# Optimization experiments

Hardware: AMD Instinct MI355X
Metric: run time of the kernel (lower is better)

The kernel has to match this reference:

```python
import jax, jax.numpy as jnp
import numpy as np

# Orthonormal (integral-normalized) real spherical harmonics, l = 0..3,
# components ordered [Y_0^0, Y_1^{-1..1}, Y_2^{-2..2}, Y_3^{-3..3}],
# with the e3nn/cuEquivariance l=1 ordering (y, z, x).
_C00 = float(0.5 * np.sqrt(1.0 / np.pi))
_C1 = float(np.sqrt(3.0 / (4.0 * np.pi)))
_C2m2 = float(0.5 * np.sqrt(15.0 / np.pi))
_C20 = float(0.25 * np.sqrt(5.0 / np.pi))
_C22 = float(0.25 * np.sqrt(15.0 / np.pi))
_C3m3 = float(0.25 * np.sqrt(35.0 / (2.0 * np.pi)))
_C3m2 = float(0.5 * np.sqrt(105.0 / np.pi))
_C3m1 = float(0.25 * np.sqrt(21.0 / (2.0 * np.pi)))
_C30 = float(0.25 * np.sqrt(7.0 / np.pi))
_C32 = float(0.25 * np.sqrt(105.0 / np.pi))

N_EDGES = 4_000_000


def setup_inputs() -> dict:
    key = jax.random.key(0)
    vectors = jax.random.normal(key, (N_EDGES, 3), dtype=jnp.float32)
    return {"vectors": vectors}


def _sh_l3(vectors):
    # normalize=True: project onto unit sphere first
    v = vectors * jax.lax.rsqrt(jnp.sum(vectors * vectors, axis=-1, keepdims=True))
    x, y, z = v[..., 0], v[..., 1], v[..., 2]
    x2, y2, z2 = x * x, y * y, z * z
    one = jnp.ones_like(x)
    ys = [
        _C00 * one,                       # l=0
        _C1 * y, _C1 * z, _C1 * x,        # l=1 (m=-1,0,1)
        _C2m2 * x * y,                    # l=2, m=-2
        _C2m2 * y * z,                    # l=2, m=-1
        _C20 * (3.0 * z2 - 1.0),          # l=2, m=0
        _C2m2 * x * z,                    # l=2, m=1
        _C22 * (x2 - y2),                 # l=2, m=2
        _C3m3 * y * (3.0 * x2 - y2),      # l=3, m=-3
        _C3m2 * x * y * z,                # l=3, m=-2
        _C3m1 * y * (5.0 * z2 - 1.0),     # l=3, m=-1
        _C30 * z * (5.0 * z2 - 3.0),      # l=3, m=0
        _C3m1 * x * (5.0 * z2 - 1.0),     # l=3, m=1
        _C32 * z * (x2 - y2),             # l=3, m=2
        _C3m3 * x * (x2 - 3.0 * y2),      # l=3, m=3
    ]
    return jnp.stack(ys, axis=-1)  # (..., 16)


def reference(vectors) -> jnp.ndarray:
    return _sh_l3(vectors)
```

## Files before the change

kernel.cpp:

```cpp
#include <hip/hip_runtime.h>

#define C00  0.28209479177387814f
#define C1   0.4886025119029199f
#define C2M2 1.0925484305920792f
#define C20  0.31539156525252005f
#define C22  0.5462742152960396f
#define C3M3 0.5900435899266435f
#define C3M2 2.890611442640554f
#define C3M1 0.4570457994644658f
#define C30  0.3731763325901154f
#define C32  1.445305721320277f

typedef float vfloat4 __attribute__((ext_vector_type(4)));

#define PITCH 260

__global__ __launch_bounds__(256) void sh_l3_kernel(
    const float* __restrict__ v, float* __restrict__ out) {
    __shared__ float sh[16][PITCH];

    const int t = threadIdx.x;
    const unsigned gbase = blockIdx.x * 256u;
    const unsigned edge = gbase + t;

    const float* p = v + 3ull * edge;
    float x = p[0], y = p[1], z = p[2];

    float rinv = rsqrtf(x * x + y * y + z * z);
    x *= rinv; y *= rinv; z *= rinv;

    float x2 = x * x, y2 = y * y, z2 = z * z;

    sh[0][t]  = C00;
    sh[1][t]  = C1 * y;
    sh[2][t]  = C1 * z;
    sh[3][t]  = C1 * x;
    sh[4][t]  = C2M2 * x * y;
    sh[5][t]  = C2M2 * y * z;
    sh[6][t]  = C20 * (3.0f * z2 - 1.0f);
    sh[7][t]  = C2M2 * x * z;
    sh[8][t]  = C22 * (x2 - y2);
    sh[9][t]  = C3M3 * y * (3.0f * x2 - y2);
    sh[10][t] = C3M2 * x * y * z;
    sh[11][t] = C3M1 * y * (5.0f * z2 - 1.0f);
    sh[12][t] = C30 * z * (5.0f * z2 - 3.0f);
    sh[13][t] = C3M1 * x * (5.0f * z2 - 1.0f);
    sh[14][t] = C32 * z * (x2 - y2);
    sh[15][t] = C3M3 * x * (x2 - 3.0f * y2);

    __syncthreads();

    vfloat4* out4 = reinterpret_cast<vfloat4*>(out) + 4ull * gbase;
    #pragma unroll
    for (int k = 0; k < 4; ++k) {
        unsigned idx4 = k * 256u + t;
        unsigned e  = idx4 >> 2;
        unsigned c  = (idx4 & 3u) * 4u;
        vfloat4 w;
        w.x = sh[c + 0][e];
        w.y = sh[c + 1][e];
        w.z = sh[c + 2][e];
        w.w = sh[c + 3][e];
        __builtin_nontemporal_store(w, &out4[idx4]);
    }
}

extern "C" void kernel_launch(void* const* d_in, const int* in_sizes, int n_in,
                              void* d_out, int out_size, void* d_ws, size_t ws_size,
                              hipStream_t stream) {
    const float* v = (const float*)d_in[0];
    float* out = (float*)d_out;
    int n = in_sizes[0] / 3;
    int grid = n / 256;
    sh_l3_kernel<<<grid, 256, 0, stream>>>(v, out);
}
```

Before: 284.7 us.

## Stage input through LDS with vector loads and store outputs directly per thread

The kernel now loads each block's 768 input floats with 192 coalesced float4 loads into shared memory, replacing the stride-3 scalar loads. The output shared-memory transpose is removed, and each thread writes its 16 outputs as four consecutive float4 nontemporal stores. This swaps the output staging for input staging, keeping one barrier while cutting LDS traffic. The per-thread 64-byte stores are not fully contiguous across a wavefront per instruction, though each wavefront still covers one contiguous region overall.

```diff
diff --git a/kernel.cpp b/kernel.cpp
--- a/kernel.cpp
+++ b/kernel.cpp
@@ -13,56 +13,53 @@
 
 typedef float vfloat4 __attribute__((ext_vector_type(4)));
 
-#define PITCH 260
-
 __global__ __launch_bounds__(256) void sh_l3_kernel(
     const float* __restrict__ v, float* __restrict__ out) {
-    __shared__ float sh[16][PITCH];
+    __shared__ float vin[768];
 
     const int t = threadIdx.x;
     const unsigned gbase = blockIdx.x * 256u;
     const unsigned edge = gbase + t;
 
-    const float* p = v + 3ull * edge;
-    float x = p[0], y = p[1], z = p[2];
+    if (t < 192) {
+        const vfloat4* vg = reinterpret_cast<const vfloat4*>(v)
+                          + 192ull * blockIdx.x;
+        reinterpret_cast<vfloat4*>(vin)[t] = vg[t];
+    }
+    __syncthreads();
+
+    float x = vin[3 * t + 0];
+    float y = vin[3 * t + 1];
+    float z = vin[3 * t + 2];
 
     float rinv = rsqrtf(x * x + y * y + z * z);
     x *= rinv; y *= rinv; z *= rinv;
 
     float x2 = x * x, y2 = y * y, z2 = z * z;
 
-    sh[0][t]  = C00;
-    sh[1][t]  = C1 * y;
-    sh[2][t]  = C1 * z;
-    sh[3][t]  = C1 * x;
-    sh[4][t]  = C2M2 * x * y;
-    sh[5][t]  = C2M2 * y * z;
-    sh[6][t]  = C20 * (3.0f * z2 - 1.0f);
-    sh[7][t]  = C2M2 * x * z;
-    sh[8][t]  = C22 * (x2 - y2);
-    sh[9][t]  = C3M3 * y * (3.0f * x2 - y2);
-    sh[10][t] = C3M2 * x * y * z;
-    sh[11][t] = C3M1 * y * (5.0f * z2 - 1.0f);
-    sh[12][t] = C30 * z * (5.0f * z2 - 3.0f);
-    sh[13][t] = C3M1 * x * (5.0f * z2 - 1.0f);
-    sh[14][t] = C32 * z * (x2 - y2);
-    sh[15][t] = C3M3 * x * (x2 - 3.0f * y2);
+    vfloat4 o0, o1, o2, o3;
+    o0.x = C00;
+    o0.y = C1 * y;
+    o0.z = C1 * z;
+    o0.w = C1 * x;
+    o1.x = C2M2 * x * y;
+    o1.y = C2M2 * y * z;
+    o1.z = C20 * (3.0f * z2 - 1.0f);
+    o1.w = C2M2 * x * z;
+    o2.x = C22 * (x2 - y2);
+    o2.y = C3M3 * y * (3.0f * x2 - y2);
+    o2.z = C3M2 * x * y * z;
+    o2.w = C3M1 * y * (5.0f * z2 - 1.0f);
+    o3.x = C30 * z * (5.0f * z2 - 3.0f);
+    o3.y = C3M1 * x * (5.0f * z2 - 1.0f);
+    o3.z = C32 * z * (x2 - y2);
+    o3.w = C3M3 * x * (x2 - 3.0f * y2);
 
-    __syncthreads();
-
-    vfloat4* out4 = reinterpret_cast<vfloat4*>(out) + 4ull * gbase;
-    #pragma unroll
-    for (int k = 0; k < 4; ++k) {
-        unsigned idx4 = k * 256u + t;
-        unsigned e  = idx4 >> 2;
-        unsigned c  = (idx4 & 3u) * 4u;
-        vfloat4 w;
-        w.x = sh[c + 0][e];
-        w.y = sh[c + 1][e];
-        w.z = sh[c + 2][e];
-        w.w = sh[c + 3][e];
-        __builtin_nontemporal_store(w, &out4[idx4]);
-    }
+    vfloat4* o = reinterpret_cast<vfloat4*>(out) + 4ull * edge;
+    __builtin_nontemporal_store(o0, o + 0);
+    __builtin_nontemporal_store(o1, o + 1);
+    __builtin_nontemporal_store(o2, o + 2);
+    __builtin_nontemporal_store(o3, o + 3);
 }
 
 extern "C" void kernel_launch(void* const* d_in, const int* in_sizes, int n_in,
```

New measurement: 424.7 us. +49.2%, slower.
